# Performance work log

Measured on AMD Instinct MI355X. Metric: run time of the kernel, lower is better.

## Reference

```python
import jax, jax.numpy as jnp
import numpy as np

HID = 128
N_LAYERS = 6


def _init_linear(key, fan_in, fan_out, scale=None):
    kw, kb = jax.random.split(key)
    s = scale if scale is not None else (1.0 / np.sqrt(fan_in))
    W = jax.random.uniform(kw, (fan_in, fan_out), jnp.float32, -s, s)
    b = jnp.zeros((fan_out,), jnp.float32)
    return W, b


def setup_inputs() -> dict:
    key = jax.random.key(0)
    ks = jax.random.split(key, 16)
    N, E, EC = 50000, 600000, 100000
    x = jax.random.normal(ks[0], (N, 9), jnp.float32)
    edge_index = jax.random.randint(ks[1], (2, E), 0, N, jnp.int64)
    edge_attr = jax.random.normal(ks[2], (E, 11), jnp.float32)
    connectivity = jax.random.randint(ks[3], (EC, 2), 0, N, jnp.int64)
    bc_disp = (jax.random.uniform(ks[4], (N, 1)) < 0.1).astype(jnp.float32)
    prop_I22 = jax.random.uniform(ks[5], (EC,), jnp.float32)

    enc_W1, enc_b1 = _init_linear(ks[6], 9, HID)
    enc_W2, enc_b2 = _init_linear(ks[7], HID, HID)
    # per-layer GN params stacked along axis 0
    msg_in = 2 * HID + 11
    mk = jax.random.split(ks[8], N_LAYERS)
    uk = jax.random.split(ks[9], N_LAYERS)
    mk2 = jax.random.split(ks[10], N_LAYERS)
    msg_W1 = jnp.stack([_init_linear(mk[i], msg_in, HID)[0] for i in range(N_LAYERS)])
    msg_b1 = jnp.zeros((N_LAYERS, HID), jnp.float32)
    msg_W2 = jnp.stack([_init_linear(mk2[i], HID, HID)[0] for i in range(N_LAYERS)])
    msg_b2 = jnp.zeros((N_LAYERS, HID), jnp.float32)
    upd_W = jnp.stack([_init_linear(uk[i], 2 * HID, HID)[0] for i in range(N_LAYERS)])
    upd_b = jnp.zeros((N_LAYERS, HID), jnp.float32)

    ef_W1, ef_b1 = _init_linear(ks[11], 1 + 2 * HID, 64)
    ef_W2, ef_b2 = _init_linear(ks[12], 64, 64)
    ef_W3, ef_b3 = _init_linear(ks[13], 64, 3, scale=0.1 * np.sqrt(6.0 / (64 + 3)))

    return dict(x=x, edge_index=edge_index, edge_attr=edge_attr,
                connectivity=connectivity, bc_disp=bc_disp, prop_I22=prop_I22,
                n_quad_pts=5,
                enc_W1=enc_W1, enc_b1=enc_b1, enc_W2=enc_W2, enc_b2=enc_b2,
                msg_W1=msg_W1, msg_b1=msg_b1, msg_W2=msg_W2, msg_b2=msg_b2,
                upd_W=upd_W, upd_b=upd_b,
                ef_W1=ef_W1, ef_b1=ef_b1, ef_W2=ef_W2, ef_b2=ef_b2,
                ef_W3=ef_W3, ef_b3=ef_b3)


def reference(x, edge_index, edge_attr, connectivity, bc_disp, prop_I22, n_quad_pts,
              enc_W1, enc_b1, enc_W2, enc_b2,
              msg_W1, msg_b1, msg_W2, msg_b2, upd_W, upd_b,
              ef_W1, ef_b1, ef_W2, ef_b2, ef_W3, ef_b3):
    N = x.shape[0]
    silu = jax.nn.silu
    # encoder MLP
    h = silu(x @ enc_W1 + enc_b1)
    h = silu(h @ enc_W2 + enc_b2)
    src, dst = edge_index[0], edge_index[1]
    for l in range(N_LAYERS):
        m_in = jnp.concatenate([h[src], h[dst], edge_attr], axis=-1)  # (E, 2H+11)
        m = silu(m_in @ msg_W1[l] + msg_b1[l]) @ msg_W2[l] + msg_b2[l]
        agg = jax.ops.segment_sum(m, dst, num_segments=N)  # scatter-add
        h = jnp.concatenate([h, agg], axis=-1) @ upd_W[l] + upd_b[l] + h  # residual update
        h = silu(h)
    # continuous edge field evaluation
    n1, n2 = connectivity[:, 0], connectivity[:, 1]
    EC = connectivity.shape[0]
    xi_1d = jnp.linspace(0.0, 1.0, n_quad_pts, dtype=jnp.float32)
    xi = jnp.broadcast_to(xi_1d[None, :, None], (EC, n_quad_pts, 1))
    h_i = jnp.broadcast_to(h[n1][:, None, :], (EC, n_quad_pts, HID))
    h_j = jnp.broadcast_to(h[n2][:, None, :], (EC, n_quad_pts, HID))
    inp = jnp.concatenate([xi, h_i, h_j], axis=-1)  # (EC, n_pts, 1+2H)
    f = silu(inp @ ef_W1 + ef_b1)
    f = silu(f @ ef_W2 + ef_b2)
    fields = f @ ef_W3 + ef_b3  # (EC, n_pts, 3)
    # hard BCs
    bc_mask = bc_disp[:, 0]
    bc_i, bc_j = bc_mask[n1], bc_mask[n2]
    xi_vals = xi[..., 0]
    mask_i = 1.0 - bc_i[:, None] * (1.0 - xi_vals)
    mask_j = 1.0 - bc_j[:, None] * xi_vals
    fields = fields * (mask_i * mask_j)[..., None]
    return h, xi, fields, prop_I22
```

## Files before the change

kernel.cpp:

```cpp
#include <hip/hip_runtime.h>
#include <hip/hip_bf16.h>

#define HID 128
#define EA_DIM 11
#define MSG_IN (2 * HID + EA_DIM)
#define TILE_E 128
#define KCAP 272
#define KB (KCAP * 2)
#define MSG_LDS 139264

typedef __attribute__((ext_vector_type(8))) short short8;
typedef __attribute__((ext_vector_type(16))) float f32x16;
typedef __attribute__((ext_vector_type(4))) float float4v;

__device__ __forceinline__ float siluf(float x) { return x / (1.f + __expf(-x)); }
__device__ __forceinline__ short f2bf(float f) {
    __hip_bfloat16 h = __float2bfloat16(f);
    return *reinterpret_cast<short*>(&h);
}
__device__ __forceinline__ int crow(int r, int khalf) { return (r & 3) + 8 * (r >> 2) + 4 * khalf; }

__device__ __forceinline__ int swz(int a) { return a ^ (((a >> 7) & 7) << 4); }

__global__ __launch_bounds__(128) void encoder_kernel(
    const float* __restrict__ x, const float* __restrict__ W1, const float* __restrict__ b1,
    const float* __restrict__ W2, const float* __restrict__ b2,
    float* __restrict__ h, short* __restrict__ hb)
{
    int i = blockIdx.x, j = threadIdx.x;
    __shared__ float xs[9];
    __shared__ float t1[HID];
    if (j < 9) xs[j] = x[(size_t)i * 9 + j];
    __syncthreads();
    float acc = b1[j];
    #pragma unroll
    for (int k = 0; k < 9; ++k) acc = fmaf(xs[k], W1[k * HID + j], acc);
    t1[j] = siluf(acc);
    __syncthreads();
    float acc2 = b2[j];
    #pragma unroll 8
    for (int k = 0; k < HID; ++k) acc2 = fmaf(t1[k], W2[k * HID + j], acc2);
    float v = siluf(acc2);
    h[(size_t)i * HID + j] = v;
    if (hb) hb[(size_t)i * HID + j] = f2bf(v);
}

__global__ void convert_w_kernel(
    const float* __restrict__ msgW1, const float* __restrict__ msgW2,
    const float* __restrict__ updW,
    const float* __restrict__ efW1, const float* __restrict__ efW2, const float* __restrict__ efW3,
    short* __restrict__ w1t, short* __restrict__ w2t, short* __restrict__ updwt,
    short* __restrict__ efw1t, short* __restrict__ efw2t, short* __restrict__ efw3t, int nl)
{
    int gid = blockIdx.x * blockDim.x + threadIdx.x;
    int n1 = nl * 128 * (KCAP / 8);
    int n2 = nl * 128 * (HID / 8);
    int n3 = nl * 128 * 32;
    int n4 = 64 * 32, n5 = 64 * 8, n6 = 32 * 8;
    short8 v;
    if (gid < n1) {
        int c = gid % (KCAP / 8);
        int rem = gid / (KCAP / 8);
        int n = rem % 128, lay = rem / 128;
        #pragma unroll
        for (int j = 0; j < 8; ++j) {
            int k = c * 8 + j;
            v[j] = (k < MSG_IN) ? f2bf(msgW1[(size_t)lay * MSG_IN * HID + (size_t)k * HID + n]) : (short)0;
        }
        *(short8*)(w1t + ((size_t)lay * 128 + n) * KCAP + c * 8) = v;
    } else if (gid < n1 + n2) {
        int g = gid - n1;
        int c = g % (HID / 8);
        int rem = g / (HID / 8);
        int n = rem % 128, lay = rem / 128;
        #pragma unroll
        for (int j = 0; j < 8; ++j)
            v[j] = f2bf(msgW2[(size_t)lay * HID * HID + (size_t)(c * 8 + j) * HID + n]);
        *(short8*)(w2t + ((size_t)lay * 128 + n) * HID + c * 8) = v;
    } else if (gid < n1 + n2 + n3) {
        int g = gid - n1 - n2;
        int c = g & 31;
        int rem = g >> 5;
        int n = rem & 127, lay = rem >> 7;
        #pragma unroll
        for (int j = 0; j < 8; ++j)
            v[j] = f2bf(updW[(size_t)lay * 256 * 128 + (size_t)(c * 8 + j) * 128 + n]);
        *(short8*)(updwt + ((size_t)lay * 128 + n) * 256 + c * 8) = v;
    } else if (gid < n1 + n2 + n3 + n4) {
        int g = gid - n1 - n2 - n3;
        int c = g & 31, n = g >> 5;
        #pragma unroll
        for (int j = 0; j < 8; ++j)
            v[j] = f2bf(efW1[(size_t)(c * 8 + j + 1) * 64 + n]);
        *(short8*)(efw1t + (size_t)n * 256 + c * 8) = v;
    } else if (gid < n1 + n2 + n3 + n4 + n5) {
        int g = gid - n1 - n2 - n3 - n4;
        int c = g & 7, n = g >> 3;
        #pragma unroll
        for (int j = 0; j < 8; ++j)
            v[j] = f2bf(efW2[(size_t)(c * 8 + j) * 64 + n]);
        *(short8*)(efw2t + (size_t)n * 64 + c * 8) = v;
    } else if (gid < n1 + n2 + n3 + n4 + n5 + n6) {
        int g = gid - n1 - n2 - n3 - n4 - n5;
        int c = g & 7, n = g >> 3;
        #pragma unroll
        for (int j = 0; j < 8; ++j)
            v[j] = (n < 3) ? f2bf(efW3[(size_t)(c * 8 + j) * 3 + n]) : (short)0;
        *(short8*)(efw3t + (size_t)n * 64 + c * 8) = v;
    }
}

__global__ void hist_kernel(const int* __restrict__ ei, int* __restrict__ cnt, int E)
{
    for (int e = blockIdx.x * blockDim.x + threadIdx.x; e < E; e += gridDim.x * blockDim.x)
        atomicAdd(&cnt[ei[(size_t)E + e]], 1);
}
__global__ __launch_bounds__(256) void scanA_kernel(const int* __restrict__ cnt, int* __restrict__ btot, int N)
{
    __shared__ int s[256];
    int i = blockIdx.x * 256 + threadIdx.x;
    s[threadIdx.x] = (i < N) ? cnt[i] : 0;
    __syncthreads();
    for (int o = 128; o > 0; o >>= 1) {
        if (threadIdx.x < o) s[threadIdx.x] += s[threadIdx.x + o];
        __syncthreads();
    }
    if (threadIdx.x == 0) btot[blockIdx.x] = s[0];
}
__global__ __launch_bounds__(1024) void scanB_kernel(int* __restrict__ btot, int nb)
{
    __shared__ int s[1024];
    int t = threadIdx.x;
    int v = (t < nb) ? btot[t] : 0;
    s[t] = v;
    __syncthreads();
    for (int o = 1; o < 1024; o <<= 1) {
        int tv = 0;
        if (t >= o) tv = s[t - o];
        __syncthreads();
        s[t] += tv;
        __syncthreads();
    }
    if (t < nb) btot[t] = s[t] - v;
}
__global__ __launch_bounds__(256) void scanC_kernel(const int* __restrict__ cnt, const int* __restrict__ btot,
                                                    int* __restrict__ cur, int N)
{
    __shared__ int s[256];
    int i = blockIdx.x * 256 + threadIdx.x;
    int t = threadIdx.x;
    int v = (i < N) ? cnt[i] : 0;
    s[t] = v;
    __syncthreads();
    for (int o = 1; o < 256; o <<= 1) {
        int tv = 0;
        if (t >= o) tv = s[t - o];
        __syncthreads();
        s[t] += tv;
        __syncthreads();
    }
    if (i < N) cur[i] = btot[blockIdx.x] + s[t] - v;
}
__global__ void scatter_kernel(const int* __restrict__ ei, int* __restrict__ cur,
                               int* __restrict__ eord, int E)
{
    for (int e = blockIdx.x * blockDim.x + threadIdx.x; e < E; e += gridDim.x * blockDim.x) {
        int d = ei[(size_t)E + e];
        int p = atomicAdd(&cur[d], 1);
        eord[p] = e;
    }
}
__global__ void reorder_kernel(const int* __restrict__ ei, const float* __restrict__ ea,
                               const int* __restrict__ eord,
                               int* __restrict__ srcs_s, int* __restrict__ dsts_s,
                               short* __restrict__ ea_s, int E)
{
    for (int p = blockIdx.x * blockDim.x + threadIdx.x; p < E; p += gridDim.x * blockDim.x) {
        int es = eord[p];
        srcs_s[p] = ei[es];
        dsts_s[p] = ei[(size_t)E + es];
        short tv[16];
        #pragma unroll
        for (int j = 0; j < 16; ++j) tv[j] = 0;
        #pragma unroll
        for (int j = 0; j < EA_DIM; ++j) tv[j] = f2bf(ea[(size_t)es * EA_DIM + j]);
        short8 v0, v1;
        #pragma unroll
        for (int j = 0; j < 8; ++j) { v0[j] = tv[j]; v1[j] = tv[8 + j]; }
        *(short8*)(ea_s + (size_t)p * 16) = v0;
        *(short8*)(ea_s + (size_t)p * 16 + 8) = v1;
    }
}

__global__ __launch_bounds__(512, 1) void msg_mfma_kernel(
    const float* __restrict__ h, const short* __restrict__ hb,
    const int* __restrict__ ei, const float* __restrict__ ea,
    const int* __restrict__ srcs_s, const int* __restrict__ dsts_s, const short* __restrict__ ea_s,
    const short* __restrict__ w1t, const float* __restrict__ b1,
    const short* __restrict__ w2t, const float* __restrict__ b2,
    float* __restrict__ agg, int E, int ntiles)
{
    extern __shared__ char smem[];
    char* sA = smem + 69632;
    __shared__ int dsts[TILE_E];

    int tid = threadIdx.x, ln = tid & 63, wave = tid >> 6;
    int mh = wave & 1, nq4 = wave >> 1;
    int l31 = ln & 31, khalf = ln >> 5;

    {
        int row = tid & 127, grp = tid >> 7;
        for (int c = grp; c < 34; c += 4) {
            short8 v = *(const short8*)(w1t + (size_t)row * KCAP + c * 8);
            *(short8*)(smem + swz(row * KB + c * 16)) = v;
        }
    }

    int col = nq4 * 32 + l31;
    float b1v = b1[col], b2v = b2[col];
    short8 zer;
    #pragma unroll
    for (int j = 0; j < 8; ++j) zer[j] = 0;
    int ar0 = mh * 64 + l31;
    const short8* w2r = (const short8*)(w2t + (size_t)col * HID);

    bool sorted = (ea_s != nullptr) && (hb != nullptr);

    int pr = tid >> 2, pq = tid & 3;
    int pf_idx = 0; bool pf_valid = false;
    short8 pf_h[8];
    short8 pf_e0 = zer, pf_e1 = zer;

    if (sorted) {
        long ep = (long)blockIdx.x * TILE_E + pr;
        pf_valid = ep < E;
        pf_idx = pf_valid ? ((pq < 2) ? srcs_s[ep] : dsts_s[ep]) : 0;
        const short8* hr8 = (const short8*)(hb + (size_t)pf_idx * HID + (pq & 1) * 64);
        #pragma unroll
        for (int c = 0; c < 8; ++c) pf_h[c] = hr8[c];
        if (pq == 3 && pf_valid) {
            pf_e0 = *(const short8*)(ea_s + (size_t)ep * 16);
            pf_e1 = *(const short8*)(ea_s + (size_t)ep * 16 + 8);
        }
    }

    #pragma unroll 1
    for (int tile = blockIdx.x; tile < ntiles; tile += gridDim.x) {
        __syncthreads();

        if (sorted) {
            int dbase = (pq >> 1) * 256 + (pq & 1) * 128;
            #pragma unroll
            for (int c = 0; c < 8; ++c) {
                short8 v = pf_valid ? pf_h[c] : zer;
                *(short8*)(sA + swz(pr * KB + dbase + c * 16)) = v;
            }
            if (pq == 2) dsts[pr] = pf_valid ? pf_idx : -1;
            if (pq == 3) {
                *(short8*)(sA + swz(pr * KB + 512)) = pf_valid ? pf_e0 : zer;
                *(short8*)(sA + swz(pr * KB + 528)) = pf_valid ? pf_e1 : zer;
            }
        } else {
            int r = pr, q = pq;
            long ep = (long)tile * TILE_E + r;
            bool valid = ep < E;
            int idx = 0;
            if (valid) idx = (q < 2) ? ei[ep] : ei[(size_t)E + ep];
            int half = q & 1;
            int dbase = (q >> 1) * 256 + half * 128;
            if (hb) {
                const short8* hr8 = (const short8*)(hb + (size_t)idx * HID + half * 64);
                #pragma unroll
                for (int c = 0; c < 8; ++c) {
                    short8 v = valid ? hr8[c] : zer;
                    *(short8*)(sA + swz(r * KB + dbase + c * 16)) = v;
                }
            } else {
                const float* hr = h + (size_t)idx * HID + half * 64;
                #pragma unroll
                for (int c = 0; c < 8; ++c) {
                    short8 v = zer;
                    if (valid) {
                        float4v f0 = *(const float4v*)(hr + c * 8);
                        float4v f1 = *(const float4v*)(hr + c * 8 + 4);
                        #pragma unroll
                        for (int j = 0; j < 4; ++j) { v[j] = f2bf(f0[j]); v[4 + j] = f2bf(f1[j]); }
                    }
                    *(short8*)(sA + swz(r * KB + dbase + c * 16)) = v;
                }
            }
            if (q == 2) dsts[r] = valid ? idx : -1;
            if (q == 3) {
                short8 v0 = zer, v1 = zer;
                if (valid) {
                    short tv[16];
                    #pragma unroll
                    for (int j = 0; j < 16; ++j) tv[j] = 0;
                    #pragma unroll
                    for (int j = 0; j < EA_DIM; ++j) tv[j] = f2bf(ea[(size_t)ep * EA_DIM + j]);
                    #pragma unroll
                    for (int j = 0; j < 8; ++j) { v0[j] = tv[j]; v1[j] = tv[8 + j]; }
                }
                *(short8*)(sA + swz(r * KB + 512)) = v0;
                *(short8*)(sA + swz(r * KB + 528)) = v1;
            }
        }
        __syncthreads();

        if (sorted) {
            long ep = (long)(tile + gridDim.x) * TILE_E + pr;
            pf_valid = ep < E;
            pf_idx = pf_valid ? ((pq < 2) ? srcs_s[ep] : dsts_s[ep]) : 0;
            const short8* hr8 = (const short8*)(hb + (size_t)pf_idx * HID + (pq & 1) * 64);
            #pragma unroll
            for (int c = 0; c < 8; ++c) pf_h[c] = hr8[c];
            if (pq == 3 && pf_valid) {
                pf_e0 = *(const short8*)(ea_s + (size_t)ep * 16);
                pf_e1 = *(const short8*)(ea_s + (size_t)ep * 16 + 8);
            }
        }

        f32x16 acc1[2] = {};
        for (int kk = 0; kk < 17; ++kk) {
            int kb = kk * 32 + khalf * 16;
            short8 a0 = *(short8*)(sA + swz(ar0 * KB + kb));
            short8 a1 = *(short8*)(sA + swz((ar0 + 32) * KB + kb));
            short8 w  = *(short8*)(smem + swz(col * KB + kb));
            acc1[0] = __builtin_amdgcn_mfma_f32_32x32x16_bf16(a0, w, acc1[0], 0, 0, 0);
            acc1[1] = __builtin_amdgcn_mfma_f32_32x32x16_bf16(a1, w, acc1[1], 0, 0, 0);
        }
        __syncthreads();

        #pragma unroll
        for (int mi = 0; mi < 2; ++mi)
            #pragma unroll
            for (int r = 0; r < 16; ++r) {
                float s = siluf(acc1[mi][r] + b1v);
                int row = mh * 64 + mi * 32 + crow(r, khalf);
                *(short*)(sA + ((row * 256 + col * 2) ^ ((row & 7) << 4))) = f2bf(s);
            }
        __syncthreads();

        f32x16 acc2[2];
        #pragma unroll
        for (int mi = 0; mi < 2; ++mi)
            #pragma unroll
            for (int r = 0; r < 16; ++r) acc2[mi][r] = b2v;
        for (int kk = 0; kk < 8; ++kk) {
            int kb = kk * 32 + khalf * 16;
            short8 a0 = *(short8*)(sA + ((ar0 * 256 + kb) ^ ((ar0 & 7) << 4)));
            short8 a1 = *(short8*)(sA + (((ar0 + 32) * 256 + kb) ^ (((ar0 + 32) & 7) << 4)));
            short8 w  = w2r[kk * 2 + khalf];
            acc2[0] = __builtin_amdgcn_mfma_f32_32x32x16_bf16(a0, w, acc2[0], 0, 0, 0);
            acc2[1] = __builtin_amdgcn_mfma_f32_32x32x16_bf16(a1, w, acc2[1], 0, 0, 0);
        }

        if (sorted) {
            float s = 0.f; int dprev = -1;
            #pragma unroll
            for (int mi = 0; mi < 2; ++mi)
                #pragma unroll
                for (int r = 0; r < 16; ++r) {
                    int row = mh * 64 + mi * 32 + crow(r, khalf);
                    int d = dsts[row];
                    if (d != dprev) {
                        if (dprev >= 0) atomicAdd(agg + (size_t)dprev * HID + col, s);
                        s = 0.f; dprev = d;
                    }
                    if (d >= 0) s += acc2[mi][r];
                }
            if (dprev >= 0) atomicAdd(agg + (size_t)dprev * HID + col, s);
        } else {
            #pragma unroll
            for (int mi = 0; mi < 2; ++mi)
                #pragma unroll
                for (int r = 0; r < 16; ++r) {
                    int row = mh * 64 + mi * 32 + crow(r, khalf);
                    int d = dsts[row];
                    if (d >= 0) atomicAdd(agg + (size_t)d * HID + col, acc2[mi][r]);
                }
        }
    }
}

__global__ __launch_bounds__(256) void upd_mfma_kernel(
    float* __restrict__ h, short* __restrict__ hb, const float* __restrict__ agg,
    const short* __restrict__ updwt, const float* __restrict__ b, int N, int ntiles)
{
    __shared__ char sA[64 * 512];
    int tid = threadIdx.x, ln = tid & 63, wave = tid >> 6;
    int mhalf = wave & 1, nhalf = wave >> 1, l31 = ln & 31, khalf = ln >> 5;
    float bv[2];
    #pragma unroll
    for (int ni = 0; ni < 2; ++ni) bv[ni] = b[nhalf * 64 + ni * 32 + l31];
    short8 zer;
    #pragma unroll
    for (int j = 0; j < 8; ++j) zer[j] = 0;

    #pragma unroll 1
    for (int tile = blockIdx.x; tile < ntiles; tile += gridDim.x) {
        __syncthreads();
        {
            int r = tid >> 2, q = tid & 3;
            int node = tile * 64 + r;
            bool valid = node < N;
            if (q < 2) {
                if (hb) {
                    const short8* hr8 = (const short8*)(hb + (size_t)node * HID + (q & 1) * 64);
                    #pragma unroll
                    for (int c = 0; c < 8; ++c) {
                        short8 v = valid ? hr8[c] : zer;
                        *(short8*)(sA + ((r * 512 + (q & 1) * 128 + c * 16) ^ ((r & 7) << 4))) = v;
                    }
                } else {
                    const float* hr = h + (size_t)node * HID + (q & 1) * 64;
                    #pragma unroll
                    for (int c = 0; c < 8; ++c) {
                        short8 v = zer;
                        if (valid) {
                            float4v f0 = *(const float4v*)(hr + c * 8);
                            float4v f1 = *(const float4v*)(hr + c * 8 + 4);
                            #pragma unroll
                            for (int j = 0; j < 4; ++j) { v[j] = f2bf(f0[j]); v[4 + j] = f2bf(f1[j]); }
                        }
                        *(short8*)(sA + ((r * 512 + (q & 1) * 128 + c * 16) ^ ((r & 7) << 4))) = v;
                    }
                }
            } else {
                const float* ar = agg + (size_t)node * HID + (q & 1) * 64;
                #pragma unroll
                for (int c = 0; c < 8; ++c) {
                    short8 v = zer;
                    if (valid) {
                        float4v f0 = *(const float4v*)(ar + c * 8);
                        float4v f1 = *(const float4v*)(ar + c * 8 + 4);
                        #pragma unroll
                        for (int j = 0; j < 4; ++j) { v[j] = f2bf(f0[j]); v[4 + j] = f2bf(f1[j]); }
                    }
                    *(short8*)(sA + ((r * 512 + 256 + (q & 1) * 128 + c * 16) ^ ((r & 7) << 4))) = v;
                }
            }
        }
        __syncthreads();
        f32x16 acc[2] = {};
        int arow = mhalf * 32 + l31;
        const short* bp0 = updwt + (size_t)(nhalf * 64 + l31) * 256 + khalf * 8;
        const short* bp1 = updwt + (size_t)(nhalf * 64 + 32 + l31) * 256 + khalf * 8;
        for (int kk = 0; kk < 16; ++kk) {
            short8 a  = *(short8*)(sA + ((arow * 512 + kk * 32 + khalf * 16) ^ ((arow & 7) << 4)));
            short8 w0 = *(const short8*)(bp0 + kk * 16);
            short8 w1 = *(const short8*)(bp1 + kk * 16);
            acc[0] = __builtin_amdgcn_mfma_f32_32x32x16_bf16(a, w0, acc[0], 0, 0, 0);
            acc[1] = __builtin_amdgcn_mfma_f32_32x32x16_bf16(a, w1, acc[1], 0, 0, 0);
        }
        #pragma unroll
        for (int ni = 0; ni < 2; ++ni) {
            int col = nhalf * 64 + ni * 32 + l31;
            #pragma unroll
            for (int r = 0; r < 16; ++r) {
                int node = tile * 64 + mhalf * 32 + crow(r, khalf);
                if (node < N) {
                    float val = siluf(acc[ni][r] + bv[ni] + h[(size_t)node * HID + col]);
                    h[(size_t)node * HID + col] = val;
                    if (hb) hb[(size_t)node * HID + col] = f2bf(val);
                }
            }
        }
    }
}

__global__ __launch_bounds__(256) void fields_mfma_kernel(
    const float* __restrict__ h, const short* __restrict__ hb,
    const int* __restrict__ conn, const float* __restrict__ bc,
    const float* __restrict__ efW1, const float* __restrict__ efb1,
    const float* __restrict__ efb2, const float* __restrict__ efb3,
    const short* __restrict__ efw1t, const short* __restrict__ efw2t, const short* __restrict__ efw3t,
    float* __restrict__ f_out, int EC, int nq, int ntiles)
{
    __shared__ char sA1[64 * 512];
    __shared__ char sA2[64 * 128];
    __shared__ char sF2[64 * 128];
    __shared__ float bcis[64], bcjs[64];
    int tid = threadIdx.x, ln = tid & 63, wave = tid >> 6;
    int mhalf = wave & 1, nhalf = wave >> 1, l31 = ln & 31, khalf = ln >> 5;
    int col = nhalf * 32 + l31;
    float w1x = efW1[col];
    float b1v = efb1[col], b2v = efb2[col];
    float b3v = (l31 < 3) ? efb3[l31] : 0.f;
    float inv = (nq > 1) ? 1.f / (float)(nq - 1) : 0.f;
    short8 zer;
    #pragma unroll
    for (int j = 0; j < 8; ++j) zer[j] = 0;

    #pragma unroll 1
    for (int tile = blockIdx.x; tile < ntiles; tile += gridDim.x) {
        __syncthreads();
        {
            int r = tid >> 2, q = tid & 3;
            long p = (long)tile * 64 + r;
            bool valid = p < EC;
            int node = 0;
            if (valid) node = conn[p * 2 + (q >> 1)];
            if (q == 0) {
                bcis[r] = valid ? bc[conn[p * 2]] : 0.f;
                bcjs[r] = valid ? bc[conn[p * 2 + 1]] : 0.f;
            }
            int cbyte = (q >> 1) * 256 + (q & 1) * 128;
            if (hb) {
                const short8* hr8 = (const short8*)(hb + (size_t)node * HID + (q & 1) * 64);
                #pragma unroll
                for (int c = 0; c < 8; ++c) {
                    short8 v = valid ? hr8[c] : zer;
                    *(short8*)(sA1 + ((r * 512 + cbyte + c * 16) ^ ((r & 7) << 4))) = v;
                }
            } else {
                const float* hr = h + (size_t)node * HID + (q & 1) * 64;
                #pragma unroll
                for (int c = 0; c < 8; ++c) {
                    short8 v = zer;
                    if (valid) {
                        float4v f0 = *(const float4v*)(hr + c * 8);
                        float4v f1 = *(const float4v*)(hr + c * 8 + 4);
                        #pragma unroll
                        for (int j = 0; j < 4; ++j) { v[j] = f2bf(f0[j]); v[4 + j] = f2bf(f1[j]); }
                    }
                    *(short8*)(sA1 + ((r * 512 + cbyte + c * 16) ^ ((r & 7) << 4))) = v;
                }
            }
        }
        __syncthreads();
        f32x16 hp = {};
        int arow = mhalf * 32 + l31;
        for (int kk = 0; kk < 16; ++kk) {
            short8 a = *(short8*)(sA1 + ((arow * 512 + kk * 32 + khalf * 16) ^ ((arow & 7) << 4)));
            short8 b = *(const short8*)(efw1t + (size_t)col * 256 + kk * 16 + khalf * 8);
            hp = __builtin_amdgcn_mfma_f32_32x32x16_bf16(a, b, hp, 0, 0, 0);
        }
        #pragma unroll
        for (int r = 0; r < 16; ++r) hp[r] += b1v;

        for (int q = 0; q < nq; ++q) {
            float xi = (float)q * inv;
            #pragma unroll
            for (int r = 0; r < 16; ++r) {
                float f1 = siluf(fmaf(xi, w1x, hp[r]));
                int row = mhalf * 32 + crow(r, khalf);
                *(short*)(sA2 + ((row * 128 + col * 2) ^ ((row & 7) << 4))) = f2bf(f1);
            }
            __syncthreads();
            f32x16 f2a = {};
            for (int kk = 0; kk < 4; ++kk) {
                short8 a = *(short8*)(sA2 + ((arow * 128 + kk * 32 + khalf * 16) ^ ((l31 & 7) << 4)));
                short8 b = *(const short8*)(efw2t + (size_t)col * 64 + kk * 16 + khalf * 8);
                f2a = __builtin_amdgcn_mfma_f32_32x32x16_bf16(a, b, f2a, 0, 0, 0);
            }
            #pragma unroll
            for (int r = 0; r < 16; ++r) {
                float f2 = siluf(f2a[r] + b2v);
                int row = mhalf * 32 + crow(r, khalf);
                *(short*)(sF2 + ((row * 128 + col * 2) ^ ((row & 7) << 4))) = f2bf(f2);
            }
            __syncthreads();
            f32x16 oa = {};
            for (int kk = 0; kk < 4; ++kk) {
                short8 a = *(short8*)(sF2 + ((arow * 128 + kk * 32 + khalf * 16) ^ ((l31 & 7) << 4)));
                short8 b = *(const short8*)(efw3t + (size_t)l31 * 64 + kk * 16 + khalf * 8);
                oa = __builtin_amdgcn_mfma_f32_32x32x16_bf16(a, b, oa, 0, 0, 0);
            }
            if (nhalf == 0 && l31 < 3) {
                #pragma unroll
                for (int r = 0; r < 16; ++r) {
                    int row = mhalf * 32 + crow(r, khalf);
                    long p = (long)tile * 64 + row;
                    if (p < EC) {
                        float mask = (1.f - bcis[row] * (1.f - xi)) * (1.f - bcjs[row] * xi);
                        f_out[((size_t)p * nq + q) * 3 + l31] = (oa[r] + b3v) * mask;
                    }
                }
            }
        }
    }
}

__global__ void aux_kernel(const float* __restrict__ prop, float* __restrict__ out_p,
                           float* __restrict__ out_xi, int EC, int nq, float inv)
{
    int i = blockIdx.x * blockDim.x + threadIdx.x;
    if (i < EC) out_p[i] = prop[i];
    if (i < EC * nq) out_xi[i] = (float)(i % nq) * inv;
}

extern "C" void kernel_launch(void* const* d_in, const int* in_sizes, int n_in,
                              void* d_out, int out_size, void* d_ws, size_t ws_size,
                              hipStream_t stream) {
    const float* x     = (const float*)d_in[0];
    const int*   ei    = (const int*)d_in[1];
    const float* ea    = (const float*)d_in[2];
    const int*   conn  = (const int*)d_in[3];
    const float* bc    = (const float*)d_in[4];
    const float* prop  = (const float*)d_in[5];
    const float* encW1 = (const float*)d_in[7];
    const float* encb1 = (const float*)d_in[8];
    const float* encW2 = (const float*)d_in[9];
    const float* encb2 = (const float*)d_in[10];
    const float* msgW1 = (const float*)d_in[11];
    const float* msgb1 = (const float*)d_in[12];
    const float* msgW2 = (const float*)d_in[13];
    const float* msgb2 = (const float*)d_in[14];
    const float* updW  = (const float*)d_in[15];
    const float* updb  = (const float*)d_in[16];
    const float* efW1  = (const float*)d_in[17];
    const float* efb1  = (const float*)d_in[18];
    const float* efW2  = (const float*)d_in[19];
    const float* efb2  = (const float*)d_in[20];
    const float* efW3  = (const float*)d_in[21];
    const float* efb3  = (const float*)d_in[22];

    int N  = in_sizes[0] / 9;
    int E  = in_sizes[1] / 2;
    int EC = in_sizes[5];
    int nl = in_sizes[11] / (MSG_IN * HID);
    int nq = (int)(((long long)out_size - (long long)N * HID - EC) / (4LL * EC));

    float* out    = (float*)d_out;
    float* h      = out;
    float* out_xi = out + (size_t)N * HID;
    float* out_f  = out_xi + (size_t)EC * nq;
    float* out_p  = out_f + (size_t)EC * nq * 3;

    size_t w1t_e = (size_t)nl * 128 * KCAP;
    size_t w2t_e = (size_t)nl * 128 * HID;
    size_t updwt_e = (size_t)nl * 128 * 256;
    size_t efw1t_e = 64 * 256, efw2t_e = 64 * 64, efw3t_e = 32 * 64;
    short* w1t   = (short*)d_ws;
    short* w2t   = w1t + w1t_e;
    short* updwt = w2t + w2t_e;
    short* efw1t = updwt + updwt_e;
    short* efw2t = efw1t + efw1t_e;
    short* efw3t = efw2t + efw2t_e;
    size_t wbytes = (w1t_e + w2t_e + updwt_e + efw1t_e + efw2t_e + efw3t_e) * 2;
    wbytes = (wbytes + 255) & ~(size_t)255;
    size_t hb_bytes  = (size_t)N * HID * 2;
    size_t agg_bytes = (size_t)N * HID * 4;
    size_t sort_bytes = ((size_t)2 * N + 1024 + (size_t)3 * E) * 4 + (size_t)E * 32;

    short* hb = nullptr;
    float* agg;
    int *icnt = nullptr, *icur = nullptr, *btot = nullptr, *eord = nullptr;
    int *srcs_s = nullptr, *dsts_s = nullptr;
    short* ea_s = nullptr;
    if (ws_size >= wbytes + hb_bytes + agg_bytes + sort_bytes) {
        char* p = (char*)d_ws + wbytes;
        hb = (short*)p;      p += hb_bytes;
        agg = (float*)p;     p += agg_bytes;
        icnt = (int*)p;      p += (size_t)N * 4;
        icur = (int*)p;      p += (size_t)N * 4;
        btot = (int*)p;      p += 1024 * 4;
        eord = (int*)p;      p += (size_t)E * 4;
        srcs_s = (int*)p;    p += (size_t)E * 4;
        dsts_s = (int*)p;    p += (size_t)E * 4;
        ea_s = (short*)p;
    } else if (ws_size >= wbytes + hb_bytes + agg_bytes) {
        hb  = (short*)((char*)d_ws + wbytes);
        agg = (float*)((char*)d_ws + wbytes + hb_bytes);
    } else {
        agg = (float*)((char*)d_ws + wbytes);
    }

    hipFuncSetAttribute((const void*)msg_mfma_kernel,
                        hipFuncAttributeMaxDynamicSharedMemorySize, MSG_LDS);

    encoder_kernel<<<N, 128, 0, stream>>>(x, encW1, encb1, encW2, encb2, h, hb);

    {
        int chunks = nl * 128 * (KCAP / 8) + nl * 128 * (HID / 8) + nl * 128 * 32
                   + 64 * 32 + 64 * 8 + 32 * 8;
        convert_w_kernel<<<(chunks + 255) / 256, 256, 0, stream>>>(
            msgW1, msgW2, updW, efW1, efW2, efW3,
            w1t, w2t, updwt, efw1t, efw2t, efw3t, nl);
    }

    if (ea_s) {
        int nb = (N + 255) / 256;
        hipMemsetAsync(icnt, 0, (size_t)N * 4, stream);
        hist_kernel<<<512, 256, 0, stream>>>(ei, icnt, E);
        scanA_kernel<<<nb, 256, 0, stream>>>(icnt, btot, N);
        scanB_kernel<<<1, 1024, 0, stream>>>(btot, nb);
        scanC_kernel<<<nb, 256, 0, stream>>>(icnt, btot, icur, N);
        scatter_kernel<<<512, 256, 0, stream>>>(ei, icur, eord, E);
        reorder_kernel<<<512, 256, 0, stream>>>(ei, ea, eord, srcs_s, dsts_s, ea_s, E);
    }

    int ntiles = (E + TILE_E - 1) / TILE_E;
    int utiles = (N + 63) / 64;
    for (int l = 0; l < nl; ++l) {
        hipMemsetAsync(agg, 0, agg_bytes, stream);
        msg_mfma_kernel<<<256, 512, MSG_LDS, stream>>>(
            h, hb, ei, ea, srcs_s, dsts_s, ea_s,
            w1t + (size_t)l * 128 * KCAP, msgb1 + (size_t)l * HID,
            w2t + (size_t)l * 128 * HID,  msgb2 + (size_t)l * HID,
            agg, E, ntiles);
        upd_mfma_kernel<<<512, 256, 0, stream>>>(
            h, hb, agg, updwt + (size_t)l * 128 * 256, updb + (size_t)l * HID, N, utiles);
    }

    int ftiles = (EC + 63) / 64;
    fields_mfma_kernel<<<512, 256, 0, stream>>>(
        h, hb, conn, bc, efW1, efb1, efb2, efb3, efw1t, efw2t, efw3t,
        out_f, EC, nq, ftiles);

    float inv = (nq > 1) ? 1.f / (float)(nq - 1) : 0.f;
    aux_kernel<<<(EC * nq + 255) / 256, 256, 0, stream>>>(prop, out_p, out_xi, EC, nq, inv);
}
```

Measured before the change: 1.749 ms.

## Zero agg inside update kernel and keep bf16 residual state between layers

The update kernel now zeroes the aggregation buffer right after loading it, so only one memset is issued before the layer loop instead of one per layer. When a bf16 copy of h exists, the residual term is read from the bf16 tile already staged in LDS rather than from fp32 global memory, and the fp32 h is written only in the last layer. This removes per-layer memset launches and fp32 h traffic. In exchange the residual path now runs at bf16 precision, and correctness depends on hb being the only h the message kernel reads in intermediate layers.

Measured after the change: 1.647 ms (median of 2 runs). 1.06x faster.

```diff
diff --git a/kernel.cpp b/kernel.cpp
--- a/kernel.cpp
+++ b/kernel.cpp
@@ -17,6 +17,9 @@
 __device__ __forceinline__ short f2bf(float f) {
     __hip_bfloat16 h = __float2bfloat16(f);
     return *reinterpret_cast<short*>(&h);
+}
+__device__ __forceinline__ float bfbits2f(unsigned short u) {
+    return __uint_as_float(((unsigned)u) << 16);
 }
 __device__ __forceinline__ int crow(int r, int khalf) { return (r & 3) + 8 * (r >> 2) + 4 * khalf; }
 
@@ -384,8 +387,8 @@
 }
 
 __global__ __launch_bounds__(256) void upd_mfma_kernel(
-    float* __restrict__ h, short* __restrict__ hb, const float* __restrict__ agg,
-    const short* __restrict__ updwt, const float* __restrict__ b, int N, int ntiles)
+    float* __restrict__ h, short* __restrict__ hb, float* __restrict__ agg,
+    const short* __restrict__ updwt, const float* __restrict__ b, int N, int ntiles, int lastl)
 {
     __shared__ char sA[64 * 512];
     int tid = threadIdx.x, ln = tid & 63, wave = tid >> 6;
@@ -427,7 +430,8 @@
                     }
                 }
             } else {
-                const float* ar = agg + (size_t)node * HID + (q & 1) * 64;
+                float* ar = agg + (size_t)node * HID + (q & 1) * 64;
+                float4v z = {0.f, 0.f, 0.f, 0.f};
                 #pragma unroll
                 for (int c = 0; c < 8; ++c) {
                     short8 v = zer;
@@ -438,6 +442,13 @@
                         for (int j = 0; j < 4; ++j) { v[j] = f2bf(f0[j]); v[4 + j] = f2bf(f1[j]); }
                     }
                     *(short8*)(sA + ((r * 512 + 256 + (q & 1) * 128 + c * 16) ^ ((r & 7) << 4))) = v;
+                }
+                if (valid) {
+                    #pragma unroll
+                    for (int c = 0; c < 8; ++c) {
+                        *(float4v*)(ar + c * 8) = z;
+                        *(float4v*)(ar + c * 8 + 4) = z;
+                    }
                 }
             }
         }
@@ -458,11 +469,23 @@
             int col = nhalf * 64 + ni * 32 + l31;
             #pragma unroll
             for (int r = 0; r < 16; ++r) {
-                int node = tile * 64 + mhalf * 32 + crow(r, khalf);
+                int rloc = mhalf * 32 + crow(r, khalf);
+                int node = tile * 64 + rloc;
                 if (node < N) {
-                    float val = siluf(acc[ni][r] + bv[ni] + h[(size_t)node * HID + col]);
-                    h[(size_t)node * HID + col] = val;
-                    if (hb) hb[(size_t)node * HID + col] = f2bf(val);
+                    float hprev;
+                    if (hb) {
+                        unsigned short u = *(unsigned short*)(sA + ((rloc * 512 + col * 2) ^ ((rloc & 7) << 4)));
+                        hprev = bfbits2f(u);
+                    } else {
+                        hprev = h[(size_t)node * HID + col];
+                    }
+                    float val = siluf(acc[ni][r] + bv[ni] + hprev);
+                    if (hb) {
+                        hb[(size_t)node * HID + col] = f2bf(val);
+                        if (lastl) h[(size_t)node * HID + col] = val;
+                    } else {
+                        h[(size_t)node * HID + col] = val;
+                    }
                 }
             }
         }
@@ -693,15 +716,16 @@
 
     int ntiles = (E + TILE_E - 1) / TILE_E;
     int utiles = (N + 63) / 64;
+    hipMemsetAsync(agg, 0, agg_bytes, stream);
     for (int l = 0; l < nl; ++l) {
-        hipMemsetAsync(agg, 0, agg_bytes, stream);
         msg_mfma_kernel<<<256, 512, MSG_LDS, stream>>>(
             h, hb, ei, ea, srcs_s, dsts_s, ea_s,
             w1t + (size_t)l * 128 * KCAP, msgb1 + (size_t)l * HID,
             w2t + (size_t)l * 128 * HID,  msgb2 + (size_t)l * HID,
             agg, E, ntiles);
         upd_mfma_kernel<<<512, 256, 0, stream>>>(
-            h, hb, agg, updwt + (size_t)l * 128 * 256, updb + (size_t)l * HID, N, utiles);
+            h, hb, agg, updwt + (size_t)l * 128 * 256, updb + (size_t)l * HID, N, utiles,
+            (l == nl - 1) ? 1 : 0);
     }
 
     int ftiles = (EC + 63) / 64;
```
